# Optimization experiments

Measured on AMD Instinct MI355X. Metric: run time of the kernel, lower is better.

The kernel has to match this reference:

```python
import jax, jax.numpy as jnp
import numpy as np

NUM_ROUTING = 3  # init kwarg num_routing


def setup_inputs() -> dict:
    key = jax.random.key(0)
    k1, k2 = jax.random.split(key)
    # x: [B=128, N=1152 primary caps, C_in=8]
    x = jax.random.normal(k1, (128, 1152, 8), dtype=jnp.float32)
    # dc_w: [capsules_dim=10, num_capsules=1152, C_in=8, C_out=16]
    dc_w = jax.random.normal(k2, (10, 1152, 8, 16), dtype=jnp.float32)
    return {"x": x, "dc_w": dc_w}


def reference(x, dc_w):
    # u = x[None,:,:,None,:] @ dc_w[:,None,:,:,:]  -> [D, B, N, 1, C_out]
    u = jnp.einsum('bni,dnio->dbno', x, dc_w)[:, :, :, None, :]
    b = jnp.zeros_like(u)
    v = None
    for i in range(NUM_ROUTING):  # small fixed routing loop
        c = jax.nn.softmax(b, axis=2)                 # softmax over primary caps
        s = jnp.sum(c * u, axis=2, keepdims=True)     # [D, B, 1, 1, C_out]
        # faithful to source: norm is taken over the (singleton) axis 2,
        # so the squash coefficient is elementwise s^2 / ((1+s^2) * |s|)
        sq = s * s
        coeff = sq / ((1.0 + sq) * jnp.sqrt(sq))
        v = coeff * s
        if i != NUM_ROUTING - 1:
            b = b + jnp.sum(u * v, axis=-1, keepdims=True)  # agreement update
    return v  # [D, B, 1, 1, C_out]
```

## Files before the change

kernel.cpp:

```cpp
#include <hip/hip_runtime.h>
#include <math.h>

constexpr int NCAPS = 1152;
constexpr int CIN   = 8;
constexpr int COUT  = 16;
constexpr int BATCH = 128;
constexpr int DCAPS = 10;
constexpr int NTHREADS = 768;
constexpr int NWAVES = NTHREADS / 64;
constexpr int QPT = NCAPS * 4 / NTHREADS;

__global__ __launch_bounds__(NTHREADS, 6) void digitcaps_kernel(
    const float* __restrict__ x,
    const float* __restrict__ w,
    float* __restrict__ out)
{
    __shared__ float4 red[NWAVES][4];
    __shared__ float  sbuf[NWAVES];
    __shared__ float4 vsh[4];

    const int i   = blockIdx.x;
    const int xcd = i & 7;
    const int k   = i >> 3;
    const int d   = (xcd >> 2) * 5 + (k % 5);
    const int b   = (k / 5) * 4 + (xcd & 3);

    const int t    = threadIdx.x;
    const int wave = t >> 6;
    const int lane = t & 63;
    const int nsub = lane >> 2;
    const int oq   = lane & 3;

    const float* xb = x + (size_t)b * NCAPS * CIN;
    const float* wd = w + (size_t)d * NCAPS * CIN * COUT + oq * 4;

    float4 u4[QPT];
    #pragma unroll
    for (int j = 0; j < QPT; ++j) {
        const int n = j * 192 + wave * 16 + nsub;
        const float4* xr = (const float4*)(xb + (size_t)n * CIN);
        float4 xa = xr[0];
        float4 xc = xr[1];
        const float* wr = wd + (size_t)n * CIN * COUT;
        float4 w0 = *(const float4*)(wr + 0 * COUT);
        float4 w1 = *(const float4*)(wr + 1 * COUT);
        float4 w2 = *(const float4*)(wr + 2 * COUT);
        float4 w3 = *(const float4*)(wr + 3 * COUT);
        float4 w4 = *(const float4*)(wr + 4 * COUT);
        float4 w5 = *(const float4*)(wr + 5 * COUT);
        float4 w6 = *(const float4*)(wr + 6 * COUT);
        float4 w7 = *(const float4*)(wr + 7 * COUT);
        float4 acc;
        acc.x = xa.x * w0.x; acc.y = xa.x * w0.y;
        acc.z = xa.x * w0.z; acc.w = xa.x * w0.w;
        acc.x = fmaf(xa.y, w1.x, acc.x); acc.y = fmaf(xa.y, w1.y, acc.y);
        acc.z = fmaf(xa.y, w1.z, acc.z); acc.w = fmaf(xa.y, w1.w, acc.w);
        acc.x = fmaf(xa.z, w2.x, acc.x); acc.y = fmaf(xa.z, w2.y, acc.y);
        acc.z = fmaf(xa.z, w2.z, acc.z); acc.w = fmaf(xa.z, w2.w, acc.w);
        acc.x = fmaf(xa.w, w3.x, acc.x); acc.y = fmaf(xa.w, w3.y, acc.y);
        acc.z = fmaf(xa.w, w3.z, acc.z); acc.w = fmaf(xa.w, w3.w, acc.w);
        acc.x = fmaf(xc.x, w4.x, acc.x); acc.y = fmaf(xc.x, w4.y, acc.y);
        acc.z = fmaf(xc.x, w4.z, acc.z); acc.w = fmaf(xc.x, w4.w, acc.w);
        acc.x = fmaf(xc.y, w5.x, acc.x); acc.y = fmaf(xc.y, w5.y, acc.y);
        acc.z = fmaf(xc.y, w5.z, acc.z); acc.w = fmaf(xc.y, w5.w, acc.w);
        acc.x = fmaf(xc.z, w6.x, acc.x); acc.y = fmaf(xc.z, w6.y, acc.y);
        acc.z = fmaf(xc.z, w6.z, acc.z); acc.w = fmaf(xc.z, w6.w, acc.w);
        acc.x = fmaf(xc.w, w7.x, acc.x); acc.y = fmaf(xc.w, w7.y, acc.y);
        acc.z = fmaf(xc.w, w7.z, acc.z); acc.w = fmaf(xc.w, w7.w, acc.w);
        u4[j] = acc;
    }

    float bb[QPT];
    #pragma unroll
    for (int j = 0; j < QPT; ++j) bb[j] = 0.f;

    #pragma unroll
    for (int it = 0; it < 3; ++it) {
        float4 p = {0.f, 0.f, 0.f, 0.f};
        float z = 0.f;
        if (it == 0) {
            #pragma unroll
            for (int j = 0; j < QPT; ++j) {
                p.x += u4[j].x; p.y += u4[j].y;
                p.z += u4[j].z; p.w += u4[j].w;
            }
        } else {
            float m = bb[0];
            #pragma unroll
            for (int j = 1; j < QPT; ++j) m = fmaxf(m, bb[j]);
            #pragma unroll
            for (int off = 1; off < 64; off <<= 1)
                m = fmaxf(m, __shfl_xor(m, off));
            if (lane == 0) sbuf[wave] = m;
            __syncthreads();
            float M = sbuf[0];
            #pragma unroll
            for (int wv = 1; wv < NWAVES; ++wv) M = fmaxf(M, sbuf[wv]);
            __syncthreads();
            #pragma unroll
            for (int j = 0; j < QPT; ++j) {
                float e = __expf(bb[j] - M);
                z += e;
                p.x = fmaf(e, u4[j].x, p.x);
                p.y = fmaf(e, u4[j].y, p.y);
                p.z = fmaf(e, u4[j].z, p.z);
                p.w = fmaf(e, u4[j].w, p.w);
            }
            z += __shfl_xor(z, 1);
            z += __shfl_xor(z, 2);
        }
        #pragma unroll
        for (int off = 4; off < 64; off <<= 1) {
            p.x += __shfl_xor(p.x, off);
            p.y += __shfl_xor(p.y, off);
            p.z += __shfl_xor(p.z, off);
            p.w += __shfl_xor(p.w, off);
            if (it != 0) z += __shfl_xor(z, off);
        }
        if (nsub == 0) red[wave][oq] = p;
        if (it != 0 && lane == 0) sbuf[wave] = z;
        __syncthreads();

        if (t < 4) {
            float4 s = red[0][t];
            #pragma unroll
            for (int wv = 1; wv < NWAVES; ++wv) {
                float4 r = red[wv][t];
                s.x += r.x; s.y += r.y; s.z += r.z; s.w += r.w;
            }
            float scale;
            if (it == 0) {
                scale = 1.f / (float)NCAPS;
            } else {
                float Z = sbuf[0];
                #pragma unroll
                for (int wv = 1; wv < NWAVES; ++wv) Z += sbuf[wv];
                scale = 4.f / Z;
            }
            s.x *= scale; s.y *= scale; s.z *= scale; s.w *= scale;
            float4 v;
            v.x = s.x * fabsf(s.x) / (1.f + s.x * s.x);
            v.y = s.y * fabsf(s.y) / (1.f + s.y * s.y);
            v.z = s.z * fabsf(s.z) / (1.f + s.z * s.z);
            v.w = s.w * fabsf(s.w) / (1.f + s.w * s.w);
            vsh[t] = v;
            if (it == 2)
                ((float4*)(out + ((size_t)d * BATCH + b) * COUT))[t] = v;
        }
        __syncthreads();

        if (it < 2) {
            float4 v = vsh[oq];
            #pragma unroll
            for (int j = 0; j < QPT; ++j) {
                float dotv = u4[j].x * v.x + u4[j].y * v.y +
                             u4[j].z * v.z + u4[j].w * v.w;
                dotv += __shfl_xor(dotv, 1);
                dotv += __shfl_xor(dotv, 2);
                bb[j] += dotv;
            }
        }
    }
}

extern "C" void kernel_launch(void* const* d_in, const int* in_sizes, int n_in,
                              void* d_out, int out_size, void* d_ws, size_t ws_size,
                              hipStream_t stream) {
    const float* x = (const float*)d_in[0];
    const float* w = (const float*)d_in[1];
    float* out = (float*)d_out;
    digitcaps_kernel<<<DCAPS * BATCH, NTHREADS, 0, stream>>>(x, w, out);
}
```

Baseline: 107.9 us.

## Split into u-precompute kernel with weight reuse and bf16 routing kernel

The fused kernel becomes two kernels. The first computes u once, holding each capsule's 8x16 weight slice in registers and reusing it across 16 batch rows, then writes u to workspace as bf16. The second kernel loads the packed bf16 u and runs the three routing iterations, using a separate shared buffer for the partition sum so one barrier can be dropped. This is meant to cut the repeated per-block weight reads. In exchange it adds a round trip of u through global memory, a second launch, and bf16 rounding of u, which could affect accuracy.

```diff
diff --git a/kernel.cpp b/kernel.cpp
--- a/kernel.cpp
+++ b/kernel.cpp
@@ -1,4 +1,5 @@
 #include <hip/hip_runtime.h>
+#include <hip/hip_bf16.h>
 #include <math.h>
 
 constexpr int NCAPS = 1152;
@@ -6,68 +7,92 @@
 constexpr int COUT  = 16;
 constexpr int BATCH = 128;
 constexpr int DCAPS = 10;
-constexpr int NTHREADS = 768;
-constexpr int NWAVES = NTHREADS / 64;
-constexpr int QPT = NCAPS * 4 / NTHREADS;
-
-__global__ __launch_bounds__(NTHREADS, 6) void digitcaps_kernel(
+
+__global__ __launch_bounds__(256, 1) void u_kernel(
     const float* __restrict__ x,
     const float* __restrict__ w,
+    __hip_bfloat16* __restrict__ u)
+{
+    const int i  = blockIdx.x;
+    const int bh = i & 1;
+    const int nc = (i >> 1) % 72;
+    const int d  = (i >> 1) / 72;
+
+    const int t    = threadIdx.x;
+    const int oq   = t & 3;
+    const int bgrp = (t >> 2) & 3;
+    const int nl   = t >> 4;
+    const int n    = nc * 16 + nl;
+    const int b0   = bh * 64 + bgrp * 16;
+
+    const float* wr = w + ((size_t)(d * NCAPS + n)) * (CIN * COUT) + oq * 4;
+    float4 W[CIN];
+    #pragma unroll
+    for (int ii = 0; ii < CIN; ++ii)
+        W[ii] = *(const float4*)(wr + ii * COUT);
+
+    const float* xp = x + ((size_t)b0 * NCAPS + n) * CIN;
+    __hip_bfloat16* up = u + ((size_t)(d * BATCH + b0) * NCAPS + n) * COUT + oq * 4;
+
+    #pragma unroll
+    for (int bi = 0; bi < 16; ++bi) {
+        const float4* xr = (const float4*)(xp + (size_t)bi * NCAPS * CIN);
+        float4 xa = xr[0], xc = xr[1];
+        float xs[CIN] = {xa.x, xa.y, xa.z, xa.w, xc.x, xc.y, xc.z, xc.w};
+        float4 acc = {0.f, 0.f, 0.f, 0.f};
+        #pragma unroll
+        for (int ii = 0; ii < CIN; ++ii) {
+            acc.x = fmaf(xs[ii], W[ii].x, acc.x);
+            acc.y = fmaf(xs[ii], W[ii].y, acc.y);
+            acc.z = fmaf(xs[ii], W[ii].z, acc.z);
+            acc.w = fmaf(xs[ii], W[ii].w, acc.w);
+        }
+        union { unsigned short us[4]; uint2 v; } pk;
+        pk.us[0] = __bfloat16_as_ushort(__float2bfloat16(acc.x));
+        pk.us[1] = __bfloat16_as_ushort(__float2bfloat16(acc.y));
+        pk.us[2] = __bfloat16_as_ushort(__float2bfloat16(acc.z));
+        pk.us[3] = __bfloat16_as_ushort(__float2bfloat16(acc.w));
+        *(uint2*)(up + (size_t)bi * NCAPS * COUT) = pk.v;
+    }
+}
+
+constexpr int BNT    = 512;
+constexpr int BWAVES = BNT / 64;
+constexpr int QPT    = NCAPS * 4 / BNT;
+
+__global__ __launch_bounds__(BNT, 1) void routing_kernel(
+    const __hip_bfloat16* __restrict__ u,
     float* __restrict__ out)
 {
-    __shared__ float4 red[NWAVES][4];
-    __shared__ float  sbuf[NWAVES];
+    __shared__ float4 red[BWAVES][4];
+    __shared__ float  sbuf[BWAVES];
+    __shared__ float  zbuf[BWAVES];
     __shared__ float4 vsh[4];
 
-    const int i   = blockIdx.x;
-    const int xcd = i & 7;
-    const int k   = i >> 3;
-    const int d   = (xcd >> 2) * 5 + (k % 5);
-    const int b   = (k / 5) * 4 + (xcd & 3);
+    const int i = blockIdx.x;
+    const int d = i >> 7;
+    const int b = i & 127;
 
     const int t    = threadIdx.x;
     const int wave = t >> 6;
     const int lane = t & 63;
-    const int nsub = lane >> 2;
-    const int oq   = lane & 3;
-
-    const float* xb = x + (size_t)b * NCAPS * CIN;
-    const float* wd = w + (size_t)d * NCAPS * CIN * COUT + oq * 4;
+    const int oq   = t & 3;
+    const int r    = t >> 2;
+
+    const __hip_bfloat16* up =
+        u + ((size_t)(d * BATCH + b) * NCAPS) * COUT + oq * 4;
 
     float4 u4[QPT];
     #pragma unroll
     for (int j = 0; j < QPT; ++j) {
-        const int n = j * 192 + wave * 16 + nsub;
-        const float4* xr = (const float4*)(xb + (size_t)n * CIN);
-        float4 xa = xr[0];
-        float4 xc = xr[1];
-        const float* wr = wd + (size_t)n * CIN * COUT;
-        float4 w0 = *(const float4*)(wr + 0 * COUT);
-        float4 w1 = *(const float4*)(wr + 1 * COUT);
-        float4 w2 = *(const float4*)(wr + 2 * COUT);
-        float4 w3 = *(const float4*)(wr + 3 * COUT);
-        float4 w4 = *(const float4*)(wr + 4 * COUT);
-        float4 w5 = *(const float4*)(wr + 5 * COUT);
-        float4 w6 = *(const float4*)(wr + 6 * COUT);
-        float4 w7 = *(const float4*)(wr + 7 * COUT);
-        float4 acc;
-        acc.x = xa.x * w0.x; acc.y = xa.x * w0.y;
-        acc.z = xa.x * w0.z; acc.w = xa.x * w0.w;
-        acc.x = fmaf(xa.y, w1.x, acc.x); acc.y = fmaf(xa.y, w1.y, acc.y);
-        acc.z = fmaf(xa.y, w1.z, acc.z); acc.w = fmaf(xa.y, w1.w, acc.w);
-        acc.x = fmaf(xa.z, w2.x, acc.x); acc.y = fmaf(xa.z, w2.y, acc.y);
-        acc.z = fmaf(xa.z, w2.z, acc.z); acc.w = fmaf(xa.z, w2.w, acc.w);
-        acc.x = fmaf(xa.w, w3.x, acc.x); acc.y = fmaf(xa.w, w3.y, acc.y);
-        acc.z = fmaf(xa.w, w3.z, acc.z); acc.w = fmaf(xa.w, w3.w, acc.w);
-        acc.x = fmaf(xc.x, w4.x, acc.x); acc.y = fmaf(xc.x, w4.y, acc.y);
-        acc.z = fmaf(xc.x, w4.z, acc.z); acc.w = fmaf(xc.x, w4.w, acc.w);
-        acc.x = fmaf(xc.y, w5.x, acc.x); acc.y = fmaf(xc.y, w5.y, acc.y);
-        acc.z = fmaf(xc.y, w5.z, acc.z); acc.w = fmaf(xc.y, w5.w, acc.w);
-        acc.x = fmaf(xc.z, w6.x, acc.x); acc.y = fmaf(xc.z, w6.y, acc.y);
-        acc.z = fmaf(xc.z, w6.z, acc.z); acc.w = fmaf(xc.z, w6.w, acc.w);
-        acc.x = fmaf(xc.w, w7.x, acc.x); acc.y = fmaf(xc.w, w7.y, acc.y);
-        acc.z = fmaf(xc.w, w7.z, acc.z); acc.w = fmaf(xc.w, w7.w, acc.w);
-        u4[j] = acc;
+        const int n = j * 128 + r;
+        uint2 pv = *(const uint2*)(up + (size_t)n * COUT);
+        float4 uf;
+        uf.x = __uint_as_float(pv.x << 16);
+        uf.y = __uint_as_float(pv.x & 0xffff0000u);
+        uf.z = __uint_as_float(pv.y << 16);
+        uf.w = __uint_as_float(pv.y & 0xffff0000u);
+        u4[j] = uf;
     }
 
     float bb[QPT];
@@ -95,8 +120,7 @@
             __syncthreads();
             float M = sbuf[0];
             #pragma unroll
-            for (int wv = 1; wv < NWAVES; ++wv) M = fmaxf(M, sbuf[wv]);
-            __syncthreads();
+            for (int wv = 1; wv < BWAVES; ++wv) M = fmaxf(M, sbuf[wv]);
             #pragma unroll
             for (int j = 0; j < QPT; ++j) {
                 float e = __expf(bb[j] - M);
@@ -117,24 +141,24 @@
             p.w += __shfl_xor(p.w, off);
             if (it != 0) z += __shfl_xor(z, off);
         }
-        if (nsub == 0) red[wave][oq] = p;
-        if (it != 0 && lane == 0) sbuf[wave] = z;
+        if (lane < 4) red[wave][oq] = p;
+        if (it != 0 && lane == 0) zbuf[wave] = z;
         __syncthreads();
 
         if (t < 4) {
             float4 s = red[0][t];
             #pragma unroll
-            for (int wv = 1; wv < NWAVES; ++wv) {
-                float4 r = red[wv][t];
-                s.x += r.x; s.y += r.y; s.z += r.z; s.w += r.w;
+            for (int wv = 1; wv < BWAVES; ++wv) {
+                float4 rr = red[wv][t];
+                s.x += rr.x; s.y += rr.y; s.z += rr.z; s.w += rr.w;
             }
             float scale;
             if (it == 0) {
                 scale = 1.f / (float)NCAPS;
             } else {
-                float Z = sbuf[0];
+                float Z = zbuf[0];
                 #pragma unroll
-                for (int wv = 1; wv < NWAVES; ++wv) Z += sbuf[wv];
+                for (int wv = 1; wv < BWAVES; ++wv) Z += zbuf[wv];
                 scale = 4.f / Z;
             }
             s.x *= scale; s.y *= scale; s.z *= scale; s.w *= scale;
@@ -169,5 +193,8 @@
     const float* x = (const float*)d_in[0];
     const float* w = (const float*)d_in[1];
     float* out = (float*)d_out;
-    digitcaps_kernel<<<DCAPS * BATCH, NTHREADS, 0, stream>>>(x, w, out);
+    __hip_bfloat16* u = (__hip_bfloat16*)d_ws;
+
+    u_kernel<<<DCAPS * 72 * 2, 256, 0, stream>>>(x, w, u);
+    routing_kernel<<<DCAPS * BATCH, BNT, 0, stream>>>(u, out);
 }
```

Result: faster. 93.93 us (-13.0%).
